# Kernel tuning notes

Hardware: AMD Instinct MI355X
Metric: run time of the kernel (lower is better)

Reference implementation:

```python
import jax, jax.numpy as jnp
import numpy as np

BETA = 0.25
NUM_EMB = 50
EMB_DIM = 192


def setup_inputs() -> dict:
    key = jax.random.key(0)
    k1, k2 = jax.random.split(key)
    N = 262144
    inputs = jax.random.normal(k1, (N, EMB_DIM), dtype=jnp.float32)
    # nn.Embedding init: uniform(-1/num_embeddings, 1/num_embeddings)
    embed_w = jax.random.uniform(k2, (NUM_EMB, EMB_DIM), dtype=jnp.float32,
                                 minval=-1.0 / NUM_EMB, maxval=1.0 / NUM_EMB)
    return {"inputs": inputs, "embed_w": embed_w}


def reference(inputs, embed_w):
    # flat_input: [N, D] (inputs already flattened to last-dim = embedding_dim)
    flat = inputs.reshape(-1, EMB_DIM)
    distances = (jnp.sum(flat * flat, axis=1, keepdims=True)
                 + jnp.sum(embed_w * embed_w, axis=1)
                 - 2.0 * (flat @ embed_w.T))
    encoding_indices = jnp.argmin(distances, axis=1)[:, None]  # [N, 1]
    # one-hot scatter + matmul in the original == direct gather of nearest code
    quantized = embed_w[encoding_indices[:, 0]]  # [N, D]
    sg = jax.lax.stop_gradient
    commitloss = (jnp.mean((sg(quantized) - flat) ** 2)
                  + BETA * jnp.mean((quantized - sg(flat)) ** 2))
    # straight-through estimator
    quantized_st = flat + sg(quantized - flat)
    contrastloss = jnp.float32(0.0)
    return (quantized_st, encoding_indices, commitloss, contrastloss)
```

## Files before the change

### kernel.cpp

```cpp
#include <hip/hip_runtime.h>
#include <cfloat>

#define NUM_EMB 50
#define EMB_DIM 192
#define ESTRIDE 196

__device__ __forceinline__ float np_tree8(const float r[8]) {
#pragma clang fp contract(off)
    return ((r[0] + r[1]) + (r[2] + r[3])) + ((r[4] + r[5]) + (r[6] + r[7]));
}

__device__ float np_sumsq_192(const float* __restrict__ p) {
#pragma clang fp contract(off)
    float tot[2];
#pragma unroll
    for (int h = 0; h < 2; ++h) {
        float r[8];
#pragma unroll
        for (int l = 0; l < 8; ++l) r[l] = 0.f;
        const float* q = p + h * 96;
        for (int t = 0; t < 12; ++t)
#pragma unroll
            for (int l = 0; l < 8; ++l) {
                float v = q[t * 8 + l];
                float pr = v * v;
                r[l] = r[l] + pr;
            }
        tot[h] = np_tree8(r);
    }
    return tot[0] + tot[1];
}

__global__ __launch_bounds__(256, 2) void vq_fused(
    const float* __restrict__ x, const float* __restrict__ ew,
    float* __restrict__ out_q, float* __restrict__ out_idx,
    float* __restrict__ out_loss, int N)
{
    __shared__ __align__(16) float sE[NUM_EMB * ESTRIDE];
    __shared__ float sB[NUM_EMB];

    for (int i = threadIdx.x; i < NUM_EMB * EMB_DIM; i += blockDim.x) {
        int k = i / EMB_DIM, j = i - k * EMB_DIM;
        sE[k * ESTRIDE + j] = ew[i];
    }
    __syncthreads();
    if (threadIdx.x < NUM_EMB)
        sB[threadIdx.x] = np_sumsq_192(&sE[threadIdx.x * ESTRIDE]);
    __syncthreads();

    const int r0 = blockIdx.x * blockDim.x + threadIdx.x;
    const int half = N >> 1;
    const float4* xg0 = (const float4*)(x + (size_t)r0 * EMB_DIM);
    const float4* xg1 = (const float4*)(x + (size_t)(r0 + half) * EMB_DIM);

    float acc0[NUM_EMB], acc1[NUM_EMB];
#pragma unroll
    for (int k = 0; k < NUM_EMB; ++k) { acc0[k] = 0.f; acc1[k] = 0.f; }

    float rA0[8], rA1[8];
    float aHalf0[2], aHalf1[2];

#pragma unroll 1
    for (int m = 0; m < 6; ++m) {
        float4 fa[8], fb[8];
#pragma unroll
        for (int q = 0; q < 8; ++q) fa[q] = xg0[m * 8 + q];
#pragma unroll
        for (int q = 0; q < 8; ++q) fb[q] = xg1[m * 8 + q];
#pragma unroll
        for (int q = 0; q < 8; ++q)
            asm volatile("" : "+v"(fa[q].x), "+v"(fa[q].y), "+v"(fa[q].z), "+v"(fa[q].w));
#pragma unroll
        for (int q = 0; q < 8; ++q)
            asm volatile("" : "+v"(fb[q].x), "+v"(fb[q].y), "+v"(fb[q].z), "+v"(fb[q].w));

        if ((m % 3) == 0) {
#pragma unroll
            for (int l = 0; l < 8; ++l) { rA0[l] = 0.f; rA1[l] = 0.f; }
        }
        {
#pragma clang fp contract(off)
#pragma unroll
            for (int q = 0; q < 8; ++q) {
                float p0 = fa[q].x * fa[q].x; rA0[(q * 4 + 0) & 7] = rA0[(q * 4 + 0) & 7] + p0;
                float p1 = fa[q].y * fa[q].y; rA0[(q * 4 + 1) & 7] = rA0[(q * 4 + 1) & 7] + p1;
                float p2 = fa[q].z * fa[q].z; rA0[(q * 4 + 2) & 7] = rA0[(q * 4 + 2) & 7] + p2;
                float p3 = fa[q].w * fa[q].w; rA0[(q * 4 + 3) & 7] = rA0[(q * 4 + 3) & 7] + p3;
            }
#pragma unroll
            for (int q = 0; q < 8; ++q) {
                float p0 = fb[q].x * fb[q].x; rA1[(q * 4 + 0) & 7] = rA1[(q * 4 + 0) & 7] + p0;
                float p1 = fb[q].y * fb[q].y; rA1[(q * 4 + 1) & 7] = rA1[(q * 4 + 1) & 7] + p1;
                float p2 = fb[q].z * fb[q].z; rA1[(q * 4 + 2) & 7] = rA1[(q * 4 + 2) & 7] + p2;
                float p3 = fb[q].w * fb[q].w; rA1[(q * 4 + 3) & 7] = rA1[(q * 4 + 3) & 7] + p3;
            }
        }
        if ((m % 3) == 2) { aHalf0[m / 3] = np_tree8(rA0); aHalf1[m / 3] = np_tree8(rA1); }

#pragma unroll
        for (int k = 0; k < NUM_EMB; ++k) {
            const float* ek = &sE[k * ESTRIDE + m * 32];
            float4 e4[8];
#pragma unroll
            for (int h = 0; h < 8; ++h) e4[h] = *(const float4*)&ek[h * 4];
#pragma unroll
            for (int h = 0; h < 8; ++h) {
                acc0[k] = __builtin_fmaf(fa[h].x, e4[h].x, acc0[k]);
                acc0[k] = __builtin_fmaf(fa[h].y, e4[h].y, acc0[k]);
                acc0[k] = __builtin_fmaf(fa[h].z, e4[h].z, acc0[k]);
                acc0[k] = __builtin_fmaf(fa[h].w, e4[h].w, acc0[k]);
            }
#pragma unroll
            for (int h = 0; h < 8; ++h) {
                acc1[k] = __builtin_fmaf(fb[h].x, e4[h].x, acc1[k]);
                acc1[k] = __builtin_fmaf(fb[h].y, e4[h].y, acc1[k]);
                acc1[k] = __builtin_fmaf(fb[h].z, e4[h].z, acc1[k]);
                acc1[k] = __builtin_fmaf(fb[h].w, e4[h].w, acc1[k]);
            }
        }
    }

    float best0, best1; int bidx0, bidx1;
    {
#pragma clang fp contract(off)
        float a0 = aHalf0[0] + aHalf0[1];
        float a1 = aHalf1[0] + aHalf1[1];
        best0 = FLT_MAX; bidx0 = 0;
        best1 = FLT_MAX; bidx1 = 0;
#pragma unroll
        for (int k = 0; k < NUM_EMB; ++k) {
            float sb = sB[k];
            float t0 = a0 + sb;
            float u0 = 2.0f * acc0[k];
            float d0 = t0 - u0;
            if (d0 < best0) { best0 = d0; bidx0 = k; }
            float t1 = a1 + sb;
            float u1 = 2.0f * acc1[k];
            float d1 = t1 - u1;
            if (d1 < best1) { best1 = d1; bidx1 = k; }
        }
    }
    out_idx[r0] = (float)bidx0;
    out_idx[r0 + half] = (float)bidx1;

    float contrib = best0 + best1;
#pragma unroll
    for (int off = 1; off < 64; off <<= 1) contrib += __shfl_xor(contrib, off);
    if ((threadIdx.x & 63) == 0) atomicAdd(out_loss, contrib);

    {
        const int lane = threadIdx.x & 63;
        const int c = lane & 7;
        const int rr = lane >> 3;
        const int waveRow0 = r0 & ~63;
#pragma unroll
        for (int g = 0; g < 8; ++g) {
            const int kk = __shfl(bidx0, g * 8 + rr);
            const int wrow = waveRow0 + g * 8 + rr;
            float4* qrow = (float4*)(out_q + (size_t)wrow * EMB_DIM);
            const float* erow = &sE[kk * ESTRIDE];
#pragma unroll
            for (int t = 0; t < 6; ++t)
                qrow[c + 8 * t] = *(const float4*)&erow[(c + 8 * t) * 4];
        }
#pragma unroll
        for (int g = 0; g < 8; ++g) {
            const int kk = __shfl(bidx1, g * 8 + rr);
            const int wrow = waveRow0 + half + g * 8 + rr;
            float4* qrow = (float4*)(out_q + (size_t)wrow * EMB_DIM);
            const float* erow = &sE[kk * ESTRIDE];
#pragma unroll
            for (int t = 0; t < 6; ++t)
                qrow[c + 8 * t] = *(const float4*)&erow[(c + 8 * t) * 4];
        }
    }
}

__global__ void vq_init(float* out_loss) { out_loss[0] = 0.f; out_loss[1] = 0.f; }

__global__ void vq_finalize(float* __restrict__ out_loss, int N)
{
    double mean = (double)out_loss[0] / ((double)N * (double)EMB_DIM);
    out_loss[0] = (float)(1.25 * mean);
    out_loss[1] = 0.f;
}

extern "C" void kernel_launch(void* const* d_in, const int* in_sizes, int n_in,
                              void* d_out, int out_size, void* d_ws, size_t ws_size,
                              hipStream_t stream)
{
    const float* x  = (const float*)d_in[0];
    const float* ew = (const float*)d_in[1];
    const int N = in_sizes[0] / EMB_DIM;

    float* out_q    = (float*)d_out;
    float* out_idx  = out_q + (size_t)N * EMB_DIM;
    float* out_loss = out_idx + N;

    vq_init<<<1, 1, 0, stream>>>(out_loss);
    vq_fused<<<N / 512, 256, 0, stream>>>(x, ew, out_q, out_idx, out_loss, N);
    vq_finalize<<<1, 1, 0, stream>>>(out_loss, N);
}
```

Before: 384.7 us.

## Process four rows per thread with codebook split into three k-blocks

Each thread now handles four input rows instead of two, and the 50 codes are processed in three blocks of 17/17/16, re-reading the input rows once per block. Each shared-memory codebook load now feeds four rows instead of two, and splitting the code range keeps the accumulators within the register budget. The cost is reading the inputs from global memory three times per row. Blocks shrink to one 64-thread wave, and every block still loads the full codebook into LDS and computes its norms, which adds more per-block setup.

```diff
diff --git a/kernel.cpp b/kernel.cpp
--- a/kernel.cpp
+++ b/kernel.cpp
@@ -31,7 +31,154 @@
     return tot[0] + tot[1];
 }
 
-__global__ __launch_bounds__(256, 2) void vq_fused(
+#define PIN2(u, v) asm volatile("" : "+v"(u.x), "+v"(u.y), "+v"(u.z), "+v"(u.w), \
+                                      "+v"(v.x), "+v"(v.y), "+v"(v.z), "+v"(v.w))
+
+template<int K0, int KN, bool SUMSQ>
+__device__ __forceinline__ void process_kblock(
+    const float4* __restrict__ xg0, const float4* __restrict__ xg1,
+    const float4* __restrict__ xg2, const float4* __restrict__ xg3,
+    const float* __restrict__ sE, const float* __restrict__ sB,
+    float& a0, float& a1, float& a2, float& a3,
+    float& best0, float& best1, float& best2, float& best3,
+    int& bidx0, int& bidx1, int& bidx2, int& bidx3)
+{
+    float acc0[KN], acc1[KN], acc2[KN], acc3[KN];
+#pragma unroll
+    for (int ki = 0; ki < KN; ++ki) { acc0[ki] = 0.f; acc1[ki] = 0.f; acc2[ki] = 0.f; acc3[ki] = 0.f; }
+
+    float rA0[8], rA1[8], rA2[8], rA3[8];
+    float aH00, aH01, aH10, aH11, aH20, aH21, aH30, aH31;
+
+#pragma unroll 1
+    for (int m = 0; m < 6; ++m) {
+        float4 fa[8], fb[8], fc[8], fd[8];
+#pragma unroll
+        for (int q = 0; q < 8; ++q) fa[q] = xg0[m * 8 + q];
+#pragma unroll
+        for (int q = 0; q < 8; ++q) fb[q] = xg1[m * 8 + q];
+#pragma unroll
+        for (int q = 0; q < 8; ++q) fc[q] = xg2[m * 8 + q];
+#pragma unroll
+        for (int q = 0; q < 8; ++q) fd[q] = xg3[m * 8 + q];
+#pragma unroll
+        for (int q = 0; q < 8; q += 2) {
+            PIN2(fa[q], fa[q + 1]);
+            PIN2(fb[q], fb[q + 1]);
+            PIN2(fc[q], fc[q + 1]);
+            PIN2(fd[q], fd[q + 1]);
+        }
+
+        if constexpr (SUMSQ) {
+            if ((m % 3) == 0) {
+#pragma unroll
+                for (int l = 0; l < 8; ++l) { rA0[l] = 0.f; rA1[l] = 0.f; rA2[l] = 0.f; rA3[l] = 0.f; }
+            }
+            {
+#pragma clang fp contract(off)
+#pragma unroll
+                for (int q = 0; q < 8; ++q) {
+                    float p0 = fa[q].x * fa[q].x; rA0[(q * 4 + 0) & 7] = rA0[(q * 4 + 0) & 7] + p0;
+                    float p1 = fa[q].y * fa[q].y; rA0[(q * 4 + 1) & 7] = rA0[(q * 4 + 1) & 7] + p1;
+                    float p2 = fa[q].z * fa[q].z; rA0[(q * 4 + 2) & 7] = rA0[(q * 4 + 2) & 7] + p2;
+                    float p3 = fa[q].w * fa[q].w; rA0[(q * 4 + 3) & 7] = rA0[(q * 4 + 3) & 7] + p3;
+                }
+#pragma unroll
+                for (int q = 0; q < 8; ++q) {
+                    float p0 = fb[q].x * fb[q].x; rA1[(q * 4 + 0) & 7] = rA1[(q * 4 + 0) & 7] + p0;
+                    float p1 = fb[q].y * fb[q].y; rA1[(q * 4 + 1) & 7] = rA1[(q * 4 + 1) & 7] + p1;
+                    float p2 = fb[q].z * fb[q].z; rA1[(q * 4 + 2) & 7] = rA1[(q * 4 + 2) & 7] + p2;
+                    float p3 = fb[q].w * fb[q].w; rA1[(q * 4 + 3) & 7] = rA1[(q * 4 + 3) & 7] + p3;
+                }
+#pragma unroll
+                for (int q = 0; q < 8; ++q) {
+                    float p0 = fc[q].x * fc[q].x; rA2[(q * 4 + 0) & 7] = rA2[(q * 4 + 0) & 7] + p0;
+                    float p1 = fc[q].y * fc[q].y; rA2[(q * 4 + 1) & 7] = rA2[(q * 4 + 1) & 7] + p1;
+                    float p2 = fc[q].z * fc[q].z; rA2[(q * 4 + 2) & 7] = rA2[(q * 4 + 2) & 7] + p2;
+                    float p3 = fc[q].w * fc[q].w; rA2[(q * 4 + 3) & 7] = rA2[(q * 4 + 3) & 7] + p3;
+                }
+#pragma unroll
+                for (int q = 0; q < 8; ++q) {
+                    float p0 = fd[q].x * fd[q].x; rA3[(q * 4 + 0) & 7] = rA3[(q * 4 + 0) & 7] + p0;
+                    float p1 = fd[q].y * fd[q].y; rA3[(q * 4 + 1) & 7] = rA3[(q * 4 + 1) & 7] + p1;
+                    float p2 = fd[q].z * fd[q].z; rA3[(q * 4 + 2) & 7] = rA3[(q * 4 + 2) & 7] + p2;
+                    float p3 = fd[q].w * fd[q].w; rA3[(q * 4 + 3) & 7] = rA3[(q * 4 + 3) & 7] + p3;
+                }
+            }
+            if (m == 2) { aH00 = np_tree8(rA0); aH10 = np_tree8(rA1); aH20 = np_tree8(rA2); aH30 = np_tree8(rA3); }
+            if (m == 5) { aH01 = np_tree8(rA0); aH11 = np_tree8(rA1); aH21 = np_tree8(rA2); aH31 = np_tree8(rA3); }
+        }
+
+        const float* ebase = &sE[K0 * ESTRIDE + m * 32];
+#pragma unroll
+        for (int ki = 0; ki < KN; ++ki) {
+            const float* ek = ebase + ki * ESTRIDE;
+            float4 e4[8];
+#pragma unroll
+            for (int h = 0; h < 8; ++h) e4[h] = *(const float4*)&ek[h * 4];
+#pragma unroll
+            for (int h = 0; h < 8; ++h) {
+                acc0[ki] = __builtin_fmaf(fa[h].x, e4[h].x, acc0[ki]);
+                acc0[ki] = __builtin_fmaf(fa[h].y, e4[h].y, acc0[ki]);
+                acc0[ki] = __builtin_fmaf(fa[h].z, e4[h].z, acc0[ki]);
+                acc0[ki] = __builtin_fmaf(fa[h].w, e4[h].w, acc0[ki]);
+            }
+#pragma unroll
+            for (int h = 0; h < 8; ++h) {
+                acc1[ki] = __builtin_fmaf(fb[h].x, e4[h].x, acc1[ki]);
+                acc1[ki] = __builtin_fmaf(fb[h].y, e4[h].y, acc1[ki]);
+                acc1[ki] = __builtin_fmaf(fb[h].z, e4[h].z, acc1[ki]);
+                acc1[ki] = __builtin_fmaf(fb[h].w, e4[h].w, acc1[ki]);
+            }
+#pragma unroll
+            for (int h = 0; h < 8; ++h) {
+                acc2[ki] = __builtin_fmaf(fc[h].x, e4[h].x, acc2[ki]);
+                acc2[ki] = __builtin_fmaf(fc[h].y, e4[h].y, acc2[ki]);
+                acc2[ki] = __builtin_fmaf(fc[h].z, e4[h].z, acc2[ki]);
+                acc2[ki] = __builtin_fmaf(fc[h].w, e4[h].w, acc2[ki]);
+            }
+#pragma unroll
+            for (int h = 0; h < 8; ++h) {
+                acc3[ki] = __builtin_fmaf(fd[h].x, e4[h].x, acc3[ki]);
+                acc3[ki] = __builtin_fmaf(fd[h].y, e4[h].y, acc3[ki]);
+                acc3[ki] = __builtin_fmaf(fd[h].z, e4[h].z, acc3[ki]);
+                acc3[ki] = __builtin_fmaf(fd[h].w, e4[h].w, acc3[ki]);
+            }
+        }
+    }
+
+    if constexpr (SUMSQ) {
+#pragma clang fp contract(off)
+        a0 = aH00 + aH01; a1 = aH10 + aH11; a2 = aH20 + aH21; a3 = aH30 + aH31;
+    }
+
+    {
+#pragma clang fp contract(off)
+#pragma unroll
+        for (int ki = 0; ki < KN; ++ki) {
+            const int k = K0 + ki;
+            const float sb = sB[k];
+            float t0 = a0 + sb;
+            float u0 = 2.0f * acc0[ki];
+            float d0 = t0 - u0;
+            if (d0 < best0) { best0 = d0; bidx0 = k; }
+            float t1 = a1 + sb;
+            float u1 = 2.0f * acc1[ki];
+            float d1 = t1 - u1;
+            if (d1 < best1) { best1 = d1; bidx1 = k; }
+            float t2 = a2 + sb;
+            float u2 = 2.0f * acc2[ki];
+            float d2 = t2 - u2;
+            if (d2 < best2) { best2 = d2; bidx2 = k; }
+            float t3 = a3 + sb;
+            float u3 = 2.0f * acc3[ki];
+            float d3 = t3 - u3;
+            if (d3 < best3) { best3 = d3; bidx3 = k; }
+        }
+    }
+}
+
+__global__ __launch_bounds__(64, 1) void vq_fused(
     const float* __restrict__ x, const float* __restrict__ ew,
     float* __restrict__ out_q, float* __restrict__ out_idx,
     float* __restrict__ out_loss, int N)
@@ -48,130 +195,52 @@
         sB[threadIdx.x] = np_sumsq_192(&sE[threadIdx.x * ESTRIDE]);
     __syncthreads();
 
-    const int r0 = blockIdx.x * blockDim.x + threadIdx.x;
-    const int half = N >> 1;
+    const int lane = threadIdx.x;
+    const int r0 = blockIdx.x * 64 + lane;
+    const int Q = N >> 2;
     const float4* xg0 = (const float4*)(x + (size_t)r0 * EMB_DIM);
-    const float4* xg1 = (const float4*)(x + (size_t)(r0 + half) * EMB_DIM);
-
-    float acc0[NUM_EMB], acc1[NUM_EMB];
-#pragma unroll
-    for (int k = 0; k < NUM_EMB; ++k) { acc0[k] = 0.f; acc1[k] = 0.f; }
-
-    float rA0[8], rA1[8];
-    float aHalf0[2], aHalf1[2];
-
-#pragma unroll 1
-    for (int m = 0; m < 6; ++m) {
-        float4 fa[8], fb[8];
-#pragma unroll
-        for (int q = 0; q < 8; ++q) fa[q] = xg0[m * 8 + q];
-#pragma unroll
-        for (int q = 0; q < 8; ++q) fb[q] = xg1[m * 8 + q];
-#pragma unroll
-        for (int q = 0; q < 8; ++q)
-            asm volatile("" : "+v"(fa[q].x), "+v"(fa[q].y), "+v"(fa[q].z), "+v"(fa[q].w));
-#pragma unroll
-        for (int q = 0; q < 8; ++q)
-            asm volatile("" : "+v"(fb[q].x), "+v"(fb[q].y), "+v"(fb[q].z), "+v"(fb[q].w));
-
-        if ((m % 3) == 0) {
-#pragma unroll
-            for (int l = 0; l < 8; ++l) { rA0[l] = 0.f; rA1[l] = 0.f; }
-        }
-        {
-#pragma clang fp contract(off)
-#pragma unroll
-            for (int q = 0; q < 8; ++q) {
-                float p0 = fa[q].x * fa[q].x; rA0[(q * 4 + 0) & 7] = rA0[(q * 4 + 0) & 7] + p0;
-                float p1 = fa[q].y * fa[q].y; rA0[(q * 4 + 1) & 7] = rA0[(q * 4 + 1) & 7] + p1;
-                float p2 = fa[q].z * fa[q].z; rA0[(q * 4 + 2) & 7] = rA0[(q * 4 + 2) & 7] + p2;
-                float p3 = fa[q].w * fa[q].w; rA0[(q * 4 + 3) & 7] = rA0[(q * 4 + 3) & 7] + p3;
-            }
-#pragma unroll
-            for (int q = 0; q < 8; ++q) {
-                float p0 = fb[q].x * fb[q].x; rA1[(q * 4 + 0) & 7] = rA1[(q * 4 + 0) & 7] + p0;
-                float p1 = fb[q].y * fb[q].y; rA1[(q * 4 + 1) & 7] = rA1[(q * 4 + 1) & 7] + p1;
-                float p2 = fb[q].z * fb[q].z; rA1[(q * 4 + 2) & 7] = rA1[(q * 4 + 2) & 7] + p2;
-                float p3 = fb[q].w * fb[q].w; rA1[(q * 4 + 3) & 7] = rA1[(q * 4 + 3) & 7] + p3;
-            }
-        }
-        if ((m % 3) == 2) { aHalf0[m / 3] = np_tree8(rA0); aHalf1[m / 3] = np_tree8(rA1); }
-
-#pragma unroll
-        for (int k = 0; k < NUM_EMB; ++k) {
-            const float* ek = &sE[k * ESTRIDE + m * 32];
-            float4 e4[8];
-#pragma unroll
-            for (int h = 0; h < 8; ++h) e4[h] = *(const float4*)&ek[h * 4];
-#pragma unroll
-            for (int h = 0; h < 8; ++h) {
-                acc0[k] = __builtin_fmaf(fa[h].x, e4[h].x, acc0[k]);
-                acc0[k] = __builtin_fmaf(fa[h].y, e4[h].y, acc0[k]);
-                acc0[k] = __builtin_fmaf(fa[h].z, e4[h].z, acc0[k]);
-                acc0[k] = __builtin_fmaf(fa[h].w, e4[h].w, acc0[k]);
-            }
-#pragma unroll
-            for (int h = 0; h < 8; ++h) {
-                acc1[k] = __builtin_fmaf(fb[h].x, e4[h].x, acc1[k]);
-                acc1[k] = __builtin_fmaf(fb[h].y, e4[h].y, acc1[k]);
-                acc1[k] = __builtin_fmaf(fb[h].z, e4[h].z, acc1[k]);
-                acc1[k] = __builtin_fmaf(fb[h].w, e4[h].w, acc1[k]);
-            }
-        }
-    }
-
-    float best0, best1; int bidx0, bidx1;
+    const float4* xg1 = (const float4*)(x + (size_t)(r0 + Q) * EMB_DIM);
+    const float4* xg2 = (const float4*)(x + (size_t)(r0 + 2 * Q) * EMB_DIM);
+    const float4* xg3 = (const float4*)(x + (size_t)(r0 + 3 * Q) * EMB_DIM);
+
+    float a0, a1, a2, a3;
+    float best0 = FLT_MAX, best1 = FLT_MAX, best2 = FLT_MAX, best3 = FLT_MAX;
+    int bidx0 = 0, bidx1 = 0, bidx2 = 0, bidx3 = 0;
+
+    process_kblock< 0, 17, true >(xg0, xg1, xg2, xg3, sE, sB, a0, a1, a2, a3,
+                                  best0, best1, best2, best3, bidx0, bidx1, bidx2, bidx3);
+    process_kblock<17, 17, false>(xg0, xg1, xg2, xg3, sE, sB, a0, a1, a2, a3,
+                                  best0, best1, best2, best3, bidx0, bidx1, bidx2, bidx3);
+    process_kblock<34, 16, false>(xg0, xg1, xg2, xg3, sE, sB, a0, a1, a2, a3,
+                                  best0, best1, best2, best3, bidx0, bidx1, bidx2, bidx3);
+
+    out_idx[r0] = (float)bidx0;
+    out_idx[r0 + Q] = (float)bidx1;
+    out_idx[r0 + 2 * Q] = (float)bidx2;
+    out_idx[r0 + 3 * Q] = (float)bidx3;
+
+    float contrib = (best0 + best1) + (best2 + best3);
+#pragma unroll
+    for (int off = 1; off < 64; off <<= 1) contrib += __shfl_xor(contrib, off);
+    if (lane == 0) atomicAdd(out_loss, contrib);
+
     {
-#pragma clang fp contract(off)
-        float a0 = aHalf0[0] + aHalf0[1];
-        float a1 = aHalf1[0] + aHalf1[1];
-        best0 = FLT_MAX; bidx0 = 0;
-        best1 = FLT_MAX; bidx1 = 0;
-#pragma unroll
-        for (int k = 0; k < NUM_EMB; ++k) {
-            float sb = sB[k];
-            float t0 = a0 + sb;
-            float u0 = 2.0f * acc0[k];
-            float d0 = t0 - u0;
-            if (d0 < best0) { best0 = d0; bidx0 = k; }
-            float t1 = a1 + sb;
-            float u1 = 2.0f * acc1[k];
-            float d1 = t1 - u1;
-            if (d1 < best1) { best1 = d1; bidx1 = k; }
-        }
-    }
-    out_idx[r0] = (float)bidx0;
-    out_idx[r0 + half] = (float)bidx1;
-
-    float contrib = best0 + best1;
-#pragma unroll
-    for (int off = 1; off < 64; off <<= 1) contrib += __shfl_xor(contrib, off);
-    if ((threadIdx.x & 63) == 0) atomicAdd(out_loss, contrib);
-
-    {
-        const int lane = threadIdx.x & 63;
         const int c = lane & 7;
         const int rr = lane >> 3;
-        const int waveRow0 = r0 & ~63;
-#pragma unroll
-        for (int g = 0; g < 8; ++g) {
-            const int kk = __shfl(bidx0, g * 8 + rr);
-            const int wrow = waveRow0 + g * 8 + rr;
-            float4* qrow = (float4*)(out_q + (size_t)wrow * EMB_DIM);
-            const float* erow = &sE[kk * ESTRIDE];
-#pragma unroll
-            for (int t = 0; t < 6; ++t)
-                qrow[c + 8 * t] = *(const float4*)&erow[(c + 8 * t) * 4];
-        }
-#pragma unroll
-        for (int g = 0; g < 8; ++g) {
-            const int kk = __shfl(bidx1, g * 8 + rr);
-            const int wrow = waveRow0 + half + g * 8 + rr;
-            float4* qrow = (float4*)(out_q + (size_t)wrow * EMB_DIM);
-            const float* erow = &sE[kk * ESTRIDE];
-#pragma unroll
-            for (int t = 0; t < 6; ++t)
-                qrow[c + 8 * t] = *(const float4*)&erow[(c + 8 * t) * 4];
+        const int wave0 = blockIdx.x * 64;
+#pragma unroll
+        for (int qtr = 0; qtr < 4; ++qtr) {
+            const int srcIdx = (qtr == 0) ? bidx0 : (qtr == 1) ? bidx1 : (qtr == 2) ? bidx2 : bidx3;
+#pragma unroll
+            for (int g = 0; g < 8; ++g) {
+                const int kk = __shfl(srcIdx, g * 8 + rr);
+                const int wrow = wave0 + qtr * Q + g * 8 + rr;
+                float4* qrow = (float4*)(out_q + (size_t)wrow * EMB_DIM);
+                const float* erow = &sE[kk * ESTRIDE];
+#pragma unroll
+                for (int t = 0; t < 6; ++t)
+                    qrow[c + 8 * t] = *(const float4*)&erow[(c + 8 * t) * 4];
+            }
         }
     }
 }
@@ -198,6 +267,6 @@
     float* out_loss = out_idx + N;
 
     vq_init<<<1, 1, 0, stream>>>(out_loss);
-    vq_fused<<<N / 512, 256, 0, stream>>>(x, ew, out_q, out_idx, out_loss, N);
+    vq_fused<<<N / 256, 64, 0, stream>>>(x, ew, out_q, out_idx, out_loss, N);
     vq_finalize<<<1, 1, 0, stream>>>(out_loss, N);
 }
```

Measured after the change: 489.6 us. +27.3%, slower.
